# Kernel tuning notes

Measured on AMD Instinct MI355X. Metric: run time of the kernel, lower is better.

Reference implementation:

```python
import jax, jax.numpy as jnp
import numpy as np

K = 5          # involution kernel size
GC = 8         # group_channels
EPS = 1e-5     # BatchNorm eps


def _unfold(x, k):
    """torch nn.Unfold(k, dilation=1, padding=(k-1)//2, stride=1) equivalent.
    x: [B,C,H,W] -> [B, C, k*k, H, W] with channel-major ordering matching
    torch's view(b, groups, group_channels, k*k, h, w)."""
    p = (k - 1) // 2
    B, C, H, W = x.shape
    xp = jnp.pad(x, ((0, 0), (0, 0), (p, p), (p, p)))
    # fixed small loop over k*k taps (k=5 -> 25 slices)
    taps = [xp[:, :, i:i + H, j:j + W] for i in range(k) for j in range(k)]
    return jnp.stack(taps, axis=2)  # [B, C, k*k, H, W]


def involution_fwd(x, w1, b1, bn_gamma, bn_beta, bn_mean, bn_var, w2, b2):
    B, C, H, W = x.shape
    groups = C // GC
    # conv1: 1x1 conv + BN(eval) + ReLU6
    y = jnp.einsum('bchw,oc->bohw', x, w1) + b1[None, :, None, None]
    scale = bn_gamma / jnp.sqrt(bn_var + EPS)
    y = y * scale[None, :, None, None] + (bn_beta - bn_mean * scale)[None, :, None, None]
    y = jnp.clip(y, 0.0, 6.0)
    # conv2: 1x1 conv -> per-pixel kernels [B, k*k*groups, H, W]
    kern = jnp.einsum('bchw,oc->bohw', y, w2) + b2[None, :, None, None]
    kern = kern.reshape(B, groups, 1, K * K, H, W)  # broadcast over group_channels
    # unfold + weighted sum over k*k taps
    patches = _unfold(x, K).reshape(B, groups, GC, K * K, H, W)
    out = (kern * patches).sum(axis=3).reshape(B, C, H, W)
    return out


def setup_inputs() -> dict:
    key = jax.random.key(0)
    ks = jax.random.split(key, 9)
    B, C, H, W = 8, 256, 64, 64
    cr = C // 4                       # reduction_ratio = 4
    groups = C // GC                  # 32
    return {
        'x': jax.random.normal(ks[0], (B, C, H, W), jnp.float32),
        'w1': jax.random.normal(ks[1], (cr, C), jnp.float32) * 0.05,
        'b1': jax.random.normal(ks[2], (cr,), jnp.float32) * 0.05,
        'bn_gamma': jax.random.uniform(ks[3], (cr,), jnp.float32, 0.5, 1.5),
        'bn_beta': jax.random.normal(ks[4], (cr,), jnp.float32) * 0.05,
        'bn_mean': jax.random.normal(ks[5], (cr,), jnp.float32) * 0.05,
        'bn_var': jax.random.uniform(ks[6], (cr,), jnp.float32, 0.5, 1.5),
        'w2': jax.random.normal(ks[7], (K * K * groups, cr), jnp.float32) * 0.05,
        'b2': jax.random.normal(ks[8], (K * K * groups,), jnp.float32) * 0.05,
    }


def reference(x, w1, b1, bn_gamma, bn_beta, bn_mean, bn_var, w2, b2):
    return involution_fwd(x, w1, b1, bn_gamma, bn_beta, bn_mean, bn_var, w2, b2)
```

## Files before the change

### kernel.cpp

```cpp
#include <hip/hip_runtime.h>

#define BB   8
#define CC   256
#define HH   64
#define WW   64
#define CR   64
#define NG   32
#define GC   8
#define KK   25
#define HW   (HH*WW)

typedef __attribute__((ext_vector_type(8))) short short8;
typedef __attribute__((ext_vector_type(4))) float f32x4;

__device__ __forceinline__ unsigned short f2bf(float f) {
    unsigned u = __builtin_bit_cast(unsigned, f);
    u += 0x7FFFu + ((u >> 16) & 1u);
    return (unsigned short)(u >> 16);
}

__global__ __launch_bounds__(256) void prep1_kernel(
    const float* __restrict__ w1, const float* __restrict__ b1,
    const float* __restrict__ gamma, const float* __restrict__ beta,
    const float* __restrict__ mean, const float* __restrict__ var,
    unsigned short* __restrict__ w1a, float* __restrict__ b1f)
{
    int idx = blockIdx.x * 256 + threadIdx.x;
    int j  = idx & 7;
    int l  = (idx >> 3) & 63;
    int mt = (idx >> 9) & 3;
    int ki = (idx >> 11) & 7;
    int r  = mt * 16 + (l & 15);
    int c  = ki * 32 + (l >> 4) * 8 + j;
    float scale = gamma[r] * rsqrtf(var[r] + 1e-5f);
    w1a[idx] = f2bf(w1[r * CC + c] * scale);
    if (idx < CR) {
        float s = gamma[idx] * rsqrtf(var[idx] + 1e-5f);
        b1f[idx] = (b1[idx] - mean[idx]) * s + beta[idx];
    }
}

__global__ __launch_bounds__(256) void prep2_kernel(
    const float* __restrict__ w2, unsigned short* __restrict__ w2p)
{
    int idx = blockIdx.x * 256 + threadIdx.x;
    int j  = idx & 7;
    int l  = (idx >> 3) & 63;
    int ki = (idx >> 9) & 1;
    int nt = (idx >> 10) & 1;
    int g  = idx >> 11;
    int nl = nt * 16 + (l & 15);
    int k  = ki * 32 + (l >> 4) * 8 + j;
    float v = (nl < KK) ? w2[(g * KK + nl) * CR + k] : 0.0f;
    w2p[idx] = f2bf(v);
}

__global__ __launch_bounds__(256) void conv1_kernel(
    const float* __restrict__ x, const unsigned short* __restrict__ w1a,
    const float* __restrict__ b1f, unsigned short* __restrict__ ybf)
{
    const int tid  = threadIdx.x;
    const int h    = blockIdx.x;
    const int b    = blockIdx.y;
    const int lane = tid & 63;
    const int wv   = tid >> 6;
    const int l15  = lane & 15;
    const int q    = lane >> 4;
    const int px   = wv * 16 + l15;

    const float*  xc   = x + (size_t)b * CC * HW + h * WW + px;
    const short8* w1a8 = (const short8*)w1a;

    f32x4 cfr[4];
    #pragma unroll
    for (int mt = 0; mt < 4; ++mt) cfr[mt] = (f32x4){0.f, 0.f, 0.f, 0.f};

    #pragma unroll
    for (int ki = 0; ki < 8; ++ki) {
        short8 bfr;
        #pragma unroll
        for (int j = 0; j < 8; ++j) {
            float v = xc[(ki * 32 + q * 8 + j) * HW];
            bfr[j] = (short)f2bf(v);
        }
        #pragma unroll
        for (int mt = 0; mt < 4; ++mt) {
            short8 afr = w1a8[(ki * 4 + mt) * 64 + lane];
            cfr[mt] = __builtin_amdgcn_mfma_f32_16x16x32_bf16(afr, bfr, cfr[mt], 0, 0, 0);
        }
    }

    unsigned short* yb = ybf + ((size_t)(b * HH + h) * WW + px) * CR;
    #pragma unroll
    for (int mt = 0; mt < 4; ++mt) {
        #pragma unroll
        for (int rp = 0; rp < 2; ++rp) {
            float v0 = cfr[mt][rp * 2 + 0] + b1f[mt * 16 + q * 4 + rp * 2 + 0];
            float v1 = cfr[mt][rp * 2 + 1] + b1f[mt * 16 + q * 4 + rp * 2 + 1];
            v0 = fminf(fmaxf(v0, 0.0f), 6.0f);
            v1 = fminf(fmaxf(v1, 0.0f), 6.0f);
            unsigned pk = (unsigned)f2bf(v0) | ((unsigned)f2bf(v1) << 16);
            *(unsigned*)(yb + mt * 16 + q * 4 + rp * 2) = pk;
        }
    }
}

__global__ __launch_bounds__(256, 4) void invol_kernel(
    const float* __restrict__ x, const unsigned short* __restrict__ ybf,
    const unsigned short* __restrict__ w2p, const float* __restrict__ b2,
    float* __restrict__ out)
{
    __shared__ float klds[4][32 * 65];

    const int tid  = threadIdx.x;
    const int h    = blockIdx.x;
    const int b    = blockIdx.y;
    const int gq   = blockIdx.z;
    const int lane = tid & 63;
    const int wv   = __builtin_amdgcn_readfirstlane(tid >> 6);
    float* kw = klds[wv];

    const int l15 = lane & 15;
    const int q   = lane >> 4;

    short8 afr[4][2];
    const unsigned short* yb = ybf + (size_t)(b * HH + h) * WW * CR;
    #pragma unroll
    for (int mt = 0; mt < 4; ++mt)
        #pragma unroll
        for (int ki = 0; ki < 2; ++ki)
            afr[mt][ki] = *(const short8*)(yb + (mt * 16 + l15) * CR + ki * 32 + q * 8);

    int  wwc[5];
    bool val[5];
    #pragma unroll
    for (int dj = 0; dj < 5; ++dj) {
        int ww  = lane + dj - 2;
        val[dj] = (ww >= 0) && (ww < WW);
        wwc[dj] = min(max(ww, 0), WW - 1);
    }

    const short8* w2p8 = (const short8*)w2p;

    #pragma unroll 1
    for (int gl = 0; gl < 4; ++gl) {
        const int g = gq * 16 + wv * 4 + gl;

        f32x4 cfr[4][2];
        #pragma unroll
        for (int nt = 0; nt < 2; ++nt) {
            int nl = nt * 16 + l15;
            float vb = b2[g * KK + min(nl, KK - 1)];
            vb = (nl < KK) ? vb : 0.0f;
            #pragma unroll
            for (int mt = 0; mt < 4; ++mt)
                cfr[mt][nt] = (f32x4){vb, vb, vb, vb};
        }

        #pragma unroll
        for (int nt = 0; nt < 2; ++nt) {
            short8 bf0 = w2p8[((g * 2 + nt) * 2 + 0) * 64 + lane];
            short8 bf1 = w2p8[((g * 2 + nt) * 2 + 1) * 64 + lane];
            #pragma unroll
            for (int mt = 0; mt < 4; ++mt) {
                cfr[mt][nt] = __builtin_amdgcn_mfma_f32_16x16x32_bf16(
                    afr[mt][0], bf0, cfr[mt][nt], 0, 0, 0);
                cfr[mt][nt] = __builtin_amdgcn_mfma_f32_16x16x32_bf16(
                    afr[mt][1], bf1, cfr[mt][nt], 0, 0, 0);
            }
        }

        #pragma unroll
        for (int mt = 0; mt < 4; ++mt)
            #pragma unroll
            for (int nt = 0; nt < 2; ++nt) {
                int n  = nt * 16 + l15;
                int px = mt * 16 + q * 4;
                #pragma unroll
                for (int r = 0; r < 4; ++r)
                    kw[n * 65 + px + r] = cfr[mt][nt][r];
            }

        float oacc[GC];
        #pragma unroll
        for (int j = 0; j < GC; ++j) oacc[j] = 0.0f;

        const float* xg = x + (size_t)(b * CC + g * GC) * HW;
        #pragma unroll
        for (int di = 0; di < 5; ++di) {
            int hh = h + di - 2;
            if (hh >= 0 && hh < HH) {
                float ks[5];
                #pragma unroll
                for (int dj = 0; dj < 5; ++dj) {
                    float kv = kw[(di * 5 + dj) * 65 + lane];
                    ks[dj] = val[dj] ? kv : 0.0f;
                }
                #pragma unroll
                for (int j = 0; j < GC; ++j) {
                    const float* xc2 = xg + (j * HH + hh) * WW;
                    #pragma unroll
                    for (int dj = 0; dj < 5; ++dj)
                        oacc[j] = fmaf(ks[dj], xc2[wwc[dj]], oacc[j]);
                }
            }
        }

        float* oc = out + ((size_t)(b * CC + g * GC) * HH + h) * WW + lane;
        #pragma unroll
        for (int j = 0; j < GC; ++j) oc[j * HW] = oacc[j];
    }
}

extern "C" void kernel_launch(void* const* d_in, const int* in_sizes, int n_in,
                              void* d_out, int out_size, void* d_ws, size_t ws_size,
                              hipStream_t stream) {
    const float* x     = (const float*)d_in[0];
    const float* w1    = (const float*)d_in[1];
    const float* b1    = (const float*)d_in[2];
    const float* gamma = (const float*)d_in[3];
    const float* beta  = (const float*)d_in[4];
    const float* mean  = (const float*)d_in[5];
    const float* var   = (const float*)d_in[6];
    const float* w2    = (const float*)d_in[7];
    const float* b2    = (const float*)d_in[8];
    float* out = (float*)d_out;

    char* ws = (char*)d_ws;
    unsigned short* w1a = (unsigned short*)ws;
    float*          b1f = (float*)(ws + 32768);
    unsigned short* w2p = (unsigned short*)(ws + 33024);
    unsigned short* ybf = (unsigned short*)(ws + 164096);

    prep1_kernel<<<64, 256, 0, stream>>>(w1, b1, gamma, beta, mean, var, w1a, b1f);
    prep2_kernel<<<256, 256, 0, stream>>>(w2, w2p);
    conv1_kernel<<<dim3(HH, BB), 256, 0, stream>>>(x, w1a, b1f, ybf);
    invol_kernel<<<dim3(HH, BB, 2), 256, 0, stream>>>(x, ybf, w2p, b2, out);
}
```

Baseline: 132.8 us.

## Merge prep kernels, widen conv1 stores, use lane shuffles for horizontal taps

```diff
diff --git a/kernel.cpp b/kernel.cpp
--- a/kernel.cpp
+++ b/kernel.cpp
@@ -19,40 +19,41 @@
     return (unsigned short)(u >> 16);
 }
 
-__global__ __launch_bounds__(256) void prep1_kernel(
+__global__ __launch_bounds__(256) void prep_kernel(
     const float* __restrict__ w1, const float* __restrict__ b1,
     const float* __restrict__ gamma, const float* __restrict__ beta,
     const float* __restrict__ mean, const float* __restrict__ var,
-    unsigned short* __restrict__ w1a, float* __restrict__ b1f)
+    const float* __restrict__ w2,
+    unsigned short* __restrict__ w1a, float* __restrict__ b1f,
+    unsigned short* __restrict__ w2p)
 {
-    int idx = blockIdx.x * 256 + threadIdx.x;
-    int j  = idx & 7;
-    int l  = (idx >> 3) & 63;
-    int mt = (idx >> 9) & 3;
-    int ki = (idx >> 11) & 7;
-    int r  = mt * 16 + (l & 15);
-    int c  = ki * 32 + (l >> 4) * 8 + j;
-    float scale = gamma[r] * rsqrtf(var[r] + 1e-5f);
-    w1a[idx] = f2bf(w1[r * CC + c] * scale);
-    if (idx < CR) {
-        float s = gamma[idx] * rsqrtf(var[idx] + 1e-5f);
-        b1f[idx] = (b1[idx] - mean[idx]) * s + beta[idx];
-    }
-}
-
-__global__ __launch_bounds__(256) void prep2_kernel(
-    const float* __restrict__ w2, unsigned short* __restrict__ w2p)
-{
-    int idx = blockIdx.x * 256 + threadIdx.x;
-    int j  = idx & 7;
-    int l  = (idx >> 3) & 63;
-    int ki = (idx >> 9) & 1;
-    int nt = (idx >> 10) & 1;
-    int g  = idx >> 11;
-    int nl = nt * 16 + (l & 15);
-    int k  = ki * 32 + (l >> 4) * 8 + j;
-    float v = (nl < KK) ? w2[(g * KK + nl) * CR + k] : 0.0f;
-    w2p[idx] = f2bf(v);
+    int gid = blockIdx.x;
+    if (gid < 256) {
+        int idx = gid * 256 + threadIdx.x;
+        int j  = idx & 7;
+        int l  = (idx >> 3) & 63;
+        int ki = (idx >> 9) & 1;
+        int nt = (idx >> 10) & 1;
+        int g  = idx >> 11;
+        int nl = nt * 16 + (l & 15);
+        int k  = ki * 32 + (l >> 4) * 8 + j;
+        float v = (nl < KK) ? w2[(g * KK + nl) * CR + k] : 0.0f;
+        w2p[idx] = f2bf(v);
+    } else {
+        int idx = (gid - 256) * 256 + threadIdx.x;
+        int j  = idx & 7;
+        int l  = (idx >> 3) & 63;
+        int mt = (idx >> 9) & 3;
+        int ki = (idx >> 11) & 7;
+        int r  = mt * 16 + (l & 15);
+        int c  = ki * 32 + (l >> 4) * 8 + j;
+        float scale = gamma[r] * rsqrtf(var[r] + 1e-5f);
+        w1a[idx] = f2bf(w1[r * CC + c] * scale);
+        if (idx < CR) {
+            float s = gamma[idx] * rsqrtf(var[idx] + 1e-5f);
+            b1f[idx] = (b1[idx] - mean[idx]) * s + beta[idx];
+        }
+    }
 }
 
 __global__ __launch_bounds__(256) void conv1_kernel(
@@ -93,15 +94,16 @@
     unsigned short* yb = ybf + ((size_t)(b * HH + h) * WW + px) * CR;
     #pragma unroll
     for (int mt = 0; mt < 4; ++mt) {
+        unsigned pk[2];
         #pragma unroll
         for (int rp = 0; rp < 2; ++rp) {
             float v0 = cfr[mt][rp * 2 + 0] + b1f[mt * 16 + q * 4 + rp * 2 + 0];
             float v1 = cfr[mt][rp * 2 + 1] + b1f[mt * 16 + q * 4 + rp * 2 + 1];
             v0 = fminf(fmaxf(v0, 0.0f), 6.0f);
             v1 = fminf(fmaxf(v1, 0.0f), 6.0f);
-            unsigned pk = (unsigned)f2bf(v0) | ((unsigned)f2bf(v1) << 16);
-            *(unsigned*)(yb + mt * 16 + q * 4 + rp * 2) = pk;
-        }
+            pk[rp] = (unsigned)f2bf(v0) | ((unsigned)f2bf(v1) << 16);
+        }
+        *(uint2*)(yb + mt * 16 + q * 4) = make_uint2(pk[0], pk[1]);
     }
 }
 
@@ -131,13 +133,11 @@
         for (int ki = 0; ki < 2; ++ki)
             afr[mt][ki] = *(const short8*)(yb + (mt * 16 + l15) * CR + ki * 32 + q * 8);
 
-    int  wwc[5];
     bool val[5];
     #pragma unroll
     for (int dj = 0; dj < 5; ++dj) {
         int ww  = lane + dj - 2;
         val[dj] = (ww >= 0) && (ww < WW);
-        wwc[dj] = min(max(ww, 0), WW - 1);
     }
 
     const short8* w2p8 = (const short8*)w2p;
@@ -198,10 +198,16 @@
                 }
                 #pragma unroll
                 for (int j = 0; j < GC; ++j) {
-                    const float* xc2 = xg + (j * HH + hh) * WW;
-                    #pragma unroll
-                    for (int dj = 0; dj < 5; ++dj)
-                        oacc[j] = fmaf(ks[dj], xc2[wwc[dj]], oacc[j]);
+                    float xv  = xg[(j * HH + hh) * WW + lane];
+                    float xm2 = __shfl(xv, lane - 2, 64);
+                    float xm1 = __shfl(xv, lane - 1, 64);
+                    float xp1 = __shfl(xv, lane + 1, 64);
+                    float xp2 = __shfl(xv, lane + 2, 64);
+                    oacc[j] = fmaf(ks[0], xm2, oacc[j]);
+                    oacc[j] = fmaf(ks[1], xm1, oacc[j]);
+                    oacc[j] = fmaf(ks[2], xv,  oacc[j]);
+                    oacc[j] = fmaf(ks[3], xp1, oacc[j]);
+                    oacc[j] = fmaf(ks[4], xp2, oacc[j]);
                 }
             }
         }
@@ -232,8 +238,8 @@
     unsigned short* w2p = (unsigned short*)(ws + 33024);
     unsigned short* ybf = (unsigned short*)(ws + 164096);
 
-    prep1_kernel<<<64, 256, 0, stream>>>(w1, b1, gamma, beta, mean, var, w1a, b1f);
-    prep2_kernel<<<256, 256, 0, stream>>>(w2, w2p);
+    prep_kernel<<<320, 256, 0, stream>>>(w1, b1, gamma, beta, mean, var, w2,
+                                         w1a, b1f, w2p);
     conv1_kernel<<<dim3(HH, BB), 256, 0, stream>>>(x, w1a, b1f, ybf);
     invol_kernel<<<dim3(HH, BB, 2), 256, 0, stream>>>(x, ybf, w2p, b2, out);
 }
```

After: 135.5 us. +2.1%, slower.
